# Kernel optimization log

Hardware: AMD Instinct MI355X
Metric: run time of the kernel (lower is better)

Reference implementation:

```python
import jax, jax.numpy as jnp
import numpy as np

N_NODES = 100000
N_EDGES = 1600000
D_IN = 128
D_OUT = 128


def setup_inputs() -> dict:
    key = jax.random.key(0)
    k1, k2, k3, k4, k5 = jax.random.split(key, 5)
    H = jax.random.normal(k1, (N_NODES, D_IN), dtype=jnp.float32)
    vals = jax.random.uniform(k2, (N_EDGES,), dtype=jnp.float32)
    W = jax.random.normal(k3, (D_OUT, D_IN), dtype=jnp.float32) * (1.0 / np.sqrt(D_IN))
    rows = jax.random.randint(k4, (N_EDGES,), 0, N_NODES, dtype=jnp.int32)
    cols = jax.random.randint(k5, (N_EDGES,), 0, N_NODES, dtype=jnp.int32)
    return {"H": H, "vals": vals, "W": W, "rows": rows, "cols": cols}


def reference(H, vals, W, rows, cols):
    # Single-rank: communicate_fgm is a no-op (X is zeros, no remote peers).
    # SpMM: out[i] = sum_e vals[e] * H[cols[e]] for edges with rows[e] == i
    msgs = vals[:, None] * H[cols]                      # [n_edges, d_in] irregular gather
    AH = jax.ops.segment_sum(msgs, rows, num_segments=N_NODES)  # [n_nodes, d_in]
    # Linear (no bias) + ReLU
    out = jax.nn.relu(AH @ W.T)                          # [n_nodes, d_out]
    return out
```

## Files before the change

kernel.cpp:

```cpp
#include <hip/hip_runtime.h>

#define N_NODES 100000
#define N_EDGES 1600000
#define D 128
#define CAPR 48
#define NTILES 6250

#define NTHR 256
#define NBA 640
#define CHUNKA 2500
#define NCAST 64
#define NGB 1563
#define NSUP 196
#define EPC 38
#define NPL NSUP

#define WB_OFF    0u
#define HWB_OFF   65536u
#define RCNT_OFF  25669632u
#define RSLOT_OFF 26075136u
#define BCOUNT_OFF_IN_OUT 38133760u

typedef unsigned int uint;
typedef __attribute__((ext_vector_type(4))) float f32x4;
typedef __attribute__((ext_vector_type(4))) uint  u32x4;
typedef __attribute__((ext_vector_type(2))) uint  u32x2;
typedef __attribute__((ext_vector_type(2))) int   i32x2;
typedef __attribute__((ext_vector_type(4))) int   i32x4;
typedef __attribute__((ext_vector_type(8))) short bf16x8;

__device__ __forceinline__ unsigned short f2bf(float x) {
    uint u = __float_as_uint(x);
    uint r = u + 0x7fffu + ((u >> 16) & 1u);
    return (unsigned short)(r >> 16);
}

__device__ __forceinline__ void acc8(float acc[8], u32x4 q, float v) {
    acc[0] = fmaf(v, __uint_as_float(q.x << 16),         acc[0]);
    acc[1] = fmaf(v, __uint_as_float(q.x & 0xffff0000u), acc[1]);
    acc[2] = fmaf(v, __uint_as_float(q.y << 16),         acc[2]);
    acc[3] = fmaf(v, __uint_as_float(q.y & 0xffff0000u), acc[3]);
    acc[4] = fmaf(v, __uint_as_float(q.z << 16),         acc[4]);
    acc[5] = fmaf(v, __uint_as_float(q.z & 0xffff0000u), acc[5]);
    acc[6] = fmaf(v, __uint_as_float(q.w << 16),         acc[6]);
    acc[7] = fmaf(v, __uint_as_float(q.w & 0xffff0000u), acc[7]);
}

__global__ __launch_bounds__(NTHR) void k_bucketA_cast(
        const int* __restrict__ rows, const int* __restrict__ cols,
        const float* __restrict__ vals, i32x2* __restrict__ epackA,
        int* __restrict__ bcount, const float* __restrict__ W,
        unsigned short* __restrict__ Wb) {
    const int bid = blockIdx.x;
    const int tid = threadIdx.x;

    if (bid >= NBA) {
        int i = (bid - NBA) * NTHR + tid;
        Wb[i] = f2bf(W[i]);
        return;
    }

    __shared__ int hist[NSUP];
    __shared__ int cur[NSUP];
    const int e0 = bid * CHUNKA;

    if (tid < NSUP) hist[tid] = 0;
    __syncthreads();
    for (int i = tid; i < CHUNKA; i += NTHR)
        atomicAdd(&hist[rows[e0 + i] >> 9], 1);
    __syncthreads();
    if (tid < NSUP) {
        int cell = tid * NBA + bid;
        cur[tid] = cell * EPC;
        bcount[cell] = min(hist[tid], EPC);
    }
    __syncthreads();
    for (int i = tid; i < CHUNKA; i += NTHR) {
        int r = rows[e0 + i];
        int s = r >> 9;
        int p = atomicAdd(&cur[s], 1);
        if (p < (s * NBA + bid) * EPC + EPC)
            epackA[p] = (i32x2){((r & 511) << 17) | cols[e0 + i],
                                __float_as_int(vals[e0 + i])};
    }
}

__global__ __launch_bounds__(NTHR) void k_gemm_place(
        const float* __restrict__ H, const unsigned short* __restrict__ Wb,
        unsigned short* __restrict__ HWb, const i32x2* __restrict__ epackA,
        const int* __restrict__ bcount, int* __restrict__ rcnt,
        i32x2* __restrict__ rslot) {
    const int bid = blockIdx.x;
    const int tid = threadIdx.x;

    if (bid >= NGB) {
        __shared__ int cnt[512];
        const int s    = bid - NGB;
        const int g    = tid >> 4;
        const int lane = tid & 15;

        for (int i = tid; i < 512; i += NTHR) cnt[i] = 0;
        __syncthreads();
        for (int b = g; b < NBA; b += 16) {
            int idx = s * NBA + b;
            int n   = bcount[idx];
            const i32x2* src = epackA + (size_t)idx * EPC;
            for (int i = lane; i < n; i += 16) {
                i32x2 e  = src[i];
                int   lr = e.x >> 17;
                int   k  = atomicAdd(&cnt[lr], 1);
                if (k < CAPR)
                    rslot[(size_t)((s << 9) + lr) * CAPR + k] =
                        (i32x2){e.x & 0x1FFFF, e.y};
            }
        }
        __syncthreads();
        for (int i = tid; i < 512; i += NTHR) {
            int grow = (s << 9) + i;
            if (grow < N_NODES) rcnt[grow] = min(cnt[i], CAPR);
        }
        return;
    }

    const int wave = tid >> 6;
    const int lane = tid & 63;
    const int rowtile = bid * 4 + wave;
    if (rowtile >= NTILES) return;
    const int rowbase = rowtile * 16;
    const int m    = lane & 15;
    const int quad = lane >> 4;

    f32x4 acc[8];
    #pragma unroll
    for (int nt = 0; nt < 8; ++nt) acc[nt] = (f32x4){0.f, 0.f, 0.f, 0.f};

    const float* hrow = H + (size_t)(rowbase + m) * D;
    #pragma unroll
    for (int ks = 0; ks < 4; ++ks) {
        const int k0 = ks * 32 + quad * 8;
        f32x4 a0 = __builtin_nontemporal_load((const f32x4*)(hrow + k0));
        f32x4 a1 = __builtin_nontemporal_load((const f32x4*)(hrow + k0 + 4));
        bf16x8 hfr;
        hfr[0] = (short)f2bf(a0.x); hfr[1] = (short)f2bf(a0.y);
        hfr[2] = (short)f2bf(a0.z); hfr[3] = (short)f2bf(a0.w);
        hfr[4] = (short)f2bf(a1.x); hfr[5] = (short)f2bf(a1.y);
        hfr[6] = (short)f2bf(a1.z); hfr[7] = (short)f2bf(a1.w);
        #pragma unroll
        for (int nt = 0; nt < 8; ++nt) {
            bf16x8 wfr = *(const bf16x8*)(Wb + (size_t)(nt * 16 + m) * D + k0);
            acc[nt] = __builtin_amdgcn_mfma_f32_16x16x32_bf16(wfr, hfr, acc[nt], 0, 0, 0);
        }
    }

    unsigned short* orow = HWb + (size_t)(rowbase + m) * D;
    #pragma unroll
    for (int nt = 0; nt < 8; ++nt) {
        u32x2 o;
        o.x = (uint)f2bf(acc[nt][0]) | ((uint)f2bf(acc[nt][1]) << 16);
        o.y = (uint)f2bf(acc[nt][2]) | ((uint)f2bf(acc[nt][3]) << 16);
        *(u32x2*)(orow + nt * 16 + quad * 4) = o;
    }
}

__global__ __launch_bounds__(NTHR) void k_spmm2(const int* __restrict__ rcnt,
                                                const i32x2* __restrict__ rslot,
                                                const unsigned short* __restrict__ HWb,
                                                float* __restrict__ out) {
    __shared__ i32x2 sE[32][CAPR + 1];
    __shared__ int   scnt[32];
    const int tid   = threadIdx.x;
    const int lane  = tid & 15;
    const int group = tid >> 4;
    const int row0  = blockIdx.x * 32;

    #pragma unroll
    for (int rr = 0; rr < 2; ++rr) {
        int lr  = group * 2 + rr;
        int row = row0 + lr;
        int cnt = min(rcnt[row], CAPR);
        if (lane == 0) scnt[lr] = cnt;
        for (int j = lane * 2; j < cnt; j += 32) {
            i32x4 p = __builtin_nontemporal_load(
                (const i32x4*)&rslot[(size_t)row * CAPR + j]);
            sE[lr][j] = (i32x2){p.x, p.y};
            if (j + 1 < cnt) sE[lr][j + 1] = (i32x2){p.z, p.w};
        }
    }
    __syncthreads();

    const int lrA = group * 2, lrB = lrA + 1;
    const int eA = scnt[lrA], eB = scnt[lrB];

    float accA[8], accB[8];
    #pragma unroll
    for (int c = 0; c < 8; ++c) { accA[c] = 0.f; accB[c] = 0.f; }

    int jA = 0, jB = 0;
    while (jA + 3 < eA && jB + 3 < eB) {
        i32x2 a0 = sE[lrA][jA],     a1 = sE[lrA][jA + 1];
        i32x2 a2 = sE[lrA][jA + 2], a3 = sE[lrA][jA + 3];
        i32x2 b0 = sE[lrB][jB],     b1 = sE[lrB][jB + 1];
        i32x2 b2 = sE[lrB][jB + 2], b3 = sE[lrB][jB + 3];
        u32x4 qa0 = ((const u32x4*)(HWb + (size_t)a0.x * D))[lane];
        u32x4 qa1 = ((const u32x4*)(HWb + (size_t)a1.x * D))[lane];
        u32x4 qa2 = ((const u32x4*)(HWb + (size_t)a2.x * D))[lane];
        u32x4 qa3 = ((const u32x4*)(HWb + (size_t)a3.x * D))[lane];
        u32x4 qb0 = ((const u32x4*)(HWb + (size_t)b0.x * D))[lane];
        u32x4 qb1 = ((const u32x4*)(HWb + (size_t)b1.x * D))[lane];
        u32x4 qb2 = ((const u32x4*)(HWb + (size_t)b2.x * D))[lane];
        u32x4 qb3 = ((const u32x4*)(HWb + (size_t)b3.x * D))[lane];
        acc8(accA, qa0, __int_as_float(a0.y));
        acc8(accA, qa1, __int_as_float(a1.y));
        acc8(accA, qa2, __int_as_float(a2.y));
        acc8(accA, qa3, __int_as_float(a3.y));
        acc8(accB, qb0, __int_as_float(b0.y));
        acc8(accB, qb1, __int_as_float(b1.y));
        acc8(accB, qb2, __int_as_float(b2.y));
        acc8(accB, qb3, __int_as_float(b3.y));
        jA += 4; jB += 4;
    }
    for (; jA + 3 < eA; jA += 4) {
        i32x2 a0 = sE[lrA][jA],     a1 = sE[lrA][jA + 1];
        i32x2 a2 = sE[lrA][jA + 2], a3 = sE[lrA][jA + 3];
        u32x4 q0 = ((const u32x4*)(HWb + (size_t)a0.x * D))[lane];
        u32x4 q1 = ((const u32x4*)(HWb + (size_t)a1.x * D))[lane];
        u32x4 q2 = ((const u32x4*)(HWb + (size_t)a2.x * D))[lane];
        u32x4 q3 = ((const u32x4*)(HWb + (size_t)a3.x * D))[lane];
        acc8(accA, q0, __int_as_float(a0.y));
        acc8(accA, q1, __int_as_float(a1.y));
        acc8(accA, q2, __int_as_float(a2.y));
        acc8(accA, q3, __int_as_float(a3.y));
    }
    for (; jA < eA; ++jA) {
        i32x2 e = sE[lrA][jA];
        u32x4 q = ((const u32x4*)(HWb + (size_t)e.x * D))[lane];
        acc8(accA, q, __int_as_float(e.y));
    }
    for (; jB + 3 < eB; jB += 4) {
        i32x2 b0 = sE[lrB][jB],     b1 = sE[lrB][jB + 1];
        i32x2 b2 = sE[lrB][jB + 2], b3 = sE[lrB][jB + 3];
        u32x4 q0 = ((const u32x4*)(HWb + (size_t)b0.x * D))[lane];
        u32x4 q1 = ((const u32x4*)(HWb + (size_t)b1.x * D))[lane];
        u32x4 q2 = ((const u32x4*)(HWb + (size_t)b2.x * D))[lane];
        u32x4 q3 = ((const u32x4*)(HWb + (size_t)b3.x * D))[lane];
        acc8(accB, q0, __int_as_float(b0.y));
        acc8(accB, q1, __int_as_float(b1.y));
        acc8(accB, q2, __int_as_float(b2.y));
        acc8(accB, q3, __int_as_float(b3.y));
    }
    for (; jB < eB; ++jB) {
        i32x2 e = sE[lrB][jB];
        u32x4 q = ((const u32x4*)(HWb + (size_t)e.x * D))[lane];
        acc8(accB, q, __int_as_float(e.y));
    }

    const int rowA = row0 + lrA, rowB = row0 + lrB;
    f32x4 oA0 = (f32x4){fmaxf(accA[0], 0.f), fmaxf(accA[1], 0.f),
                        fmaxf(accA[2], 0.f), fmaxf(accA[3], 0.f)};
    f32x4 oA1 = (f32x4){fmaxf(accA[4], 0.f), fmaxf(accA[5], 0.f),
                        fmaxf(accA[6], 0.f), fmaxf(accA[7], 0.f)};
    f32x4 oB0 = (f32x4){fmaxf(accB[0], 0.f), fmaxf(accB[1], 0.f),
                        fmaxf(accB[2], 0.f), fmaxf(accB[3], 0.f)};
    f32x4 oB1 = (f32x4){fmaxf(accB[4], 0.f), fmaxf(accB[5], 0.f),
                        fmaxf(accB[6], 0.f), fmaxf(accB[7], 0.f)};
    __builtin_nontemporal_store(oA0, &((f32x4*)out)[rowA * 32 + lane * 2]);
    __builtin_nontemporal_store(oA1, &((f32x4*)out)[rowA * 32 + lane * 2 + 1]);
    __builtin_nontemporal_store(oB0, &((f32x4*)out)[rowB * 32 + lane * 2]);
    __builtin_nontemporal_store(oB1, &((f32x4*)out)[rowB * 32 + lane * 2 + 1]);
}

extern "C" void kernel_launch(void* const* d_in, const int* in_sizes, int n_in,
                              void* d_out, int out_size, void* d_ws, size_t ws_size,
                              hipStream_t stream) {
    const float* H    = (const float*)d_in[0];
    const float* vals = (const float*)d_in[1];
    const float* W    = (const float*)d_in[2];
    const int*   rows = (const int*)d_in[3];
    const int*   cols = (const int*)d_in[4];
    float* out = (float*)d_out;

    char* ws = (char*)d_ws;
    unsigned short* Wb     = (unsigned short*)(ws + WB_OFF);
    unsigned short* HWb    = (unsigned short*)(ws + HWB_OFF);
    int*            rcnt   = (int*)(ws + RCNT_OFF);
    i32x2*          rslot  = (i32x2*)(ws + RSLOT_OFF);
    i32x2*          epackA = (i32x2*)d_out;
    int*            bcount = (int*)((char*)d_out + BCOUNT_OFF_IN_OUT);

    k_bucketA_cast<<<NBA + NCAST, NTHR, 0, stream>>>(rows, cols, vals, epackA,
                                                     bcount, W, Wb);

    k_gemm_place<<<NGB + NPL, NTHR, 0, stream>>>(H, Wb, HWb, epackA, bcount,
                                                 rcnt, rslot);

    k_spmm2<<<N_NODES / 32, NTHR, 0, stream>>>(rcnt, rslot, HWb, out);
}
```

Before: 267.5 us.

## Use per-superbucket contiguous slots with global atomic offsets and split placement blocks

Replaces the fixed per-(block, superbucket) cell layout with one contiguous region per superbucket. Each block reserves space through a global atomicAdd on a zeroed counter. Placement blocks now scan one contiguous region, with two blocks per superbucket each handling half the local rows. This removes the per-cell count reads and scattered small segments, and doubles placement parallelism. In exchange it adds a memset launch and global atomics, each half-block reads the whole bucket, and capacity overflow is now capped per superbucket.

```diff
diff --git a/kernel.cpp b/kernel.cpp
--- a/kernel.cpp
+++ b/kernel.cpp
@@ -12,14 +12,14 @@
 #define NCAST 64
 #define NGB 1563
 #define NSUP 196
-#define EPC 38
-#define NPL NSUP
+#define SLOTA 8960
+#define NPLACE (2 * NSUP)
 
 #define WB_OFF    0u
 #define HWB_OFF   65536u
+#define SCNTA_OFF 25665536u
 #define RCNT_OFF  25669632u
 #define RSLOT_OFF 26075136u
-#define BCOUNT_OFF_IN_OUT 38133760u
 
 typedef unsigned int uint;
 typedef __attribute__((ext_vector_type(4))) float f32x4;
@@ -48,8 +48,8 @@
 
 __global__ __launch_bounds__(NTHR) void k_bucketA_cast(
         const int* __restrict__ rows, const int* __restrict__ cols,
-        const float* __restrict__ vals, i32x2* __restrict__ epackA,
-        int* __restrict__ bcount, const float* __restrict__ W,
+        const float* __restrict__ vals, int* __restrict__ scntA,
+        i32x2* __restrict__ epackA, const float* __restrict__ W,
         unsigned short* __restrict__ Wb) {
     const int bid = blockIdx.x;
     const int tid = threadIdx.x;
@@ -70,16 +70,16 @@
         atomicAdd(&hist[rows[e0 + i] >> 9], 1);
     __syncthreads();
     if (tid < NSUP) {
-        int cell = tid * NBA + bid;
-        cur[tid] = cell * EPC;
-        bcount[cell] = min(hist[tid], EPC);
+        int c = hist[tid];
+        int base = (c > 0) ? atomicAdd(&scntA[tid], c) : 0;
+        cur[tid] = tid * SLOTA + base;
     }
     __syncthreads();
     for (int i = tid; i < CHUNKA; i += NTHR) {
         int r = rows[e0 + i];
         int s = r >> 9;
         int p = atomicAdd(&cur[s], 1);
-        if (p < (s * NBA + bid) * EPC + EPC)
+        if (p < (s + 1) * SLOTA)
             epackA[p] = (i32x2){((r & 511) << 17) | cols[e0 + i],
                                 __float_as_int(vals[e0 + i])};
     }
@@ -87,38 +87,35 @@
 
 __global__ __launch_bounds__(NTHR) void k_gemm_place(
         const float* __restrict__ H, const unsigned short* __restrict__ Wb,
-        unsigned short* __restrict__ HWb, const i32x2* __restrict__ epackA,
-        const int* __restrict__ bcount, int* __restrict__ rcnt,
+        unsigned short* __restrict__ HWb, const int* __restrict__ scntA,
+        const i32x2* __restrict__ epackA, int* __restrict__ rcnt,
         i32x2* __restrict__ rslot) {
     const int bid = blockIdx.x;
     const int tid = threadIdx.x;
 
     if (bid >= NGB) {
-        __shared__ int cnt[512];
-        const int s    = bid - NGB;
-        const int g    = tid >> 4;
-        const int lane = tid & 15;
-
-        for (int i = tid; i < 512; i += NTHR) cnt[i] = 0;
+        __shared__ int cnt[NTHR];
+        const int pbid = bid - NGB;
+        const int s = pbid >> 1;
+        const int h = pbid & 1;
+        const int n = min(scntA[s], SLOTA);
+        const i32x2* src = epackA + (size_t)s * SLOTA;
+
+        cnt[tid] = 0;
         __syncthreads();
-        for (int b = g; b < NBA; b += 16) {
-            int idx = s * NBA + b;
-            int n   = bcount[idx];
-            const i32x2* src = epackA + (size_t)idx * EPC;
-            for (int i = lane; i < n; i += 16) {
-                i32x2 e  = src[i];
-                int   lr = e.x >> 17;
-                int   k  = atomicAdd(&cnt[lr], 1);
+        for (int i = tid; i < n; i += NTHR) {
+            i32x2 e  = src[i];
+            int   lr = e.x >> 17;
+            if ((lr >> 8) == h) {
+                int k = atomicAdd(&cnt[lr & 255], 1);
                 if (k < CAPR)
                     rslot[(size_t)((s << 9) + lr) * CAPR + k] =
                         (i32x2){e.x & 0x1FFFF, e.y};
             }
         }
         __syncthreads();
-        for (int i = tid; i < 512; i += NTHR) {
-            int grow = (s << 9) + i;
-            if (grow < N_NODES) rcnt[grow] = min(cnt[i], CAPR);
-        }
+        int grow = (s << 9) + (h << 8) + tid;
+        if (grow < N_NODES) rcnt[grow] = min(cnt[tid], CAPR);
         return;
     }
 
@@ -282,16 +279,18 @@
     char* ws = (char*)d_ws;
     unsigned short* Wb     = (unsigned short*)(ws + WB_OFF);
     unsigned short* HWb    = (unsigned short*)(ws + HWB_OFF);
+    int*            scntA  = (int*)(ws + SCNTA_OFF);
     int*            rcnt   = (int*)(ws + RCNT_OFF);
     i32x2*          rslot  = (i32x2*)(ws + RSLOT_OFF);
     i32x2*          epackA = (i32x2*)d_out;
-    int*            bcount = (int*)((char*)d_out + BCOUNT_OFF_IN_OUT);
-
-    k_bucketA_cast<<<NBA + NCAST, NTHR, 0, stream>>>(rows, cols, vals, epackA,
-                                                     bcount, W, Wb);
-
-    k_gemm_place<<<NGB + NPL, NTHR, 0, stream>>>(H, Wb, HWb, epackA, bcount,
-                                                 rcnt, rslot);
+
+    hipMemsetAsync(scntA, 0, NSUP * sizeof(int), stream);
+
+    k_bucketA_cast<<<NBA + NCAST, NTHR, 0, stream>>>(rows, cols, vals, scntA,
+                                                     epackA, W, Wb);
+
+    k_gemm_place<<<NGB + NPLACE, NTHR, 0, stream>>>(H, Wb, HWb, scntA, epackA,
+                                                    rcnt, rslot);
 
     k_spmm2<<<N_NODES / 32, NTHR, 0, stream>>>(rcnt, rslot, HWb, out);
 }
```

Result: faster. 252.0 us (-5.8%).
